# Kernel optimization log

Measured on AMD Instinct MI355X. Metric: run time of the kernel, lower is better.

## Reference

```python
import jax, jax.numpy as jnp
import numpy as np

N_HEAD = 16
QMIN, QMAX = 0.0, 255.0  # 8-bit asymmetric


def fake_quantize(x, scale, zp):
    # LearnableFakeQuantize (asymmetric, 8-bit) with straight-through round.
    q = x / scale + zp
    q = q + jax.lax.stop_gradient(jnp.round(q) - q)  # STE round
    q = jnp.clip(q, QMIN, QMAX)
    return (q - zp) * scale


def setup_inputs() -> dict:
    key = jax.random.key(0)
    ks = jax.random.split(key, 4)
    B, T, C = 2, 2048, 1024
    return {
        "hidden_states": jax.random.normal(ks[0], (B, T, C), jnp.float32),
        "W_attn": jax.random.normal(ks[1], (C, 3 * C), jnp.float32) * (1.0 / np.sqrt(C)),
        "b_attn": jnp.zeros((3 * C,), jnp.float32),
        "W_proj": jax.random.normal(ks[2], (C, C), jnp.float32) * (1.0 / np.sqrt(C)),
        "b_proj": jnp.zeros((C,), jnp.float32),
        "kv_scale": jnp.full((1,), 0.05, jnp.float32),
        "kv_zp": jnp.full((1,), 128.0, jnp.float32),
    }


def reference(hidden_states, W_attn, b_attn, W_proj, b_proj, kv_scale, kv_zp):
    B, T, C = hidden_states.shape
    H = N_HEAD
    D = C // H
    qkv = hidden_states @ W_attn + b_attn            # [B,T,3C]
    q, k, v = jnp.split(qkv, 3, axis=2)
    # [B,T,C] -> [B,H,T,D]
    q = q.reshape(B, T, H, D).transpose(0, 2, 1, 3)
    k = k.reshape(B, T, H, D).transpose(0, 2, 1, 3)
    v = v.reshape(B, T, H, D).transpose(0, 2, 1, 3)
    k = fake_quantize(k, kv_scale, kv_zp)
    v = fake_quantize(v, kv_scale, kv_zp)
    scores = jnp.einsum("bhqd,bhkd->bhqk", q, k) / jnp.sqrt(jnp.asarray(D, q.dtype))
    causal = jnp.tril(jnp.ones((T, T), bool))        # bias[:T,:T]
    scores = jnp.where(causal, scores, jnp.asarray(-jnp.inf, scores.dtype))
    attn = jax.nn.softmax(scores, axis=-1)
    out = jnp.einsum("bhqk,bhkd->bhqd", attn, v)     # [B,H,T,D]
    out = out.transpose(0, 2, 1, 3).reshape(B, T, C)
    return out @ W_proj + b_proj
```

## Files before the change

### kernel.cpp

```cpp
#include <hip/hip_runtime.h>
#include <math.h>

#define TB 2048
#define CC 1024
#define NH 16
#define HD 64

typedef __bf16 bf16x8 __attribute__((ext_vector_type(8)));
typedef __bf16 bf16x4 __attribute__((ext_vector_type(4)));
typedef float  f32x4  __attribute__((ext_vector_type(4)));

__device__ inline float exp2fast(float x) { return __builtin_amdgcn_exp2f(x); }

__device__ __forceinline__ void gl_lds16(const __bf16* g, __bf16* l) {
    __builtin_amdgcn_global_load_lds(
        (const __attribute__((address_space(1))) void*)g,
        (__attribute__((address_space(3))) void*)l, 16, 0, 0);
}

__global__ __launch_bounds__(256)
void prep_kernel(const float* __restrict__ hidden, __bf16* __restrict__ hb,
                 const float* __restrict__ Wa, __bf16* __restrict__ wat,
                 const float* __restrict__ Wp, __bf16* __restrict__ wpt)
{
    __shared__ __bf16 L[64][68];
    const int tid = threadIdx.x;
    const int bid = blockIdx.x;
    if (bid < 4096) {
        int i = (bid * 256 + tid) * 4;
        f32x4 v = *(const f32x4*)&hidden[i];
        bf16x4 o;
        o.x = (__bf16)v.x; o.y = (__bf16)v.y; o.z = (__bf16)v.z; o.w = (__bf16)v.w;
        *(bf16x4*)&hb[i] = o;
        return;
    }
    const float* src; __bf16* dst; int N, n0, k0;
    if (bid < 4096 + 768) {
        int t = bid - 4096;
        src = Wa; dst = wat; N = 3072;
        n0 = (t % 48) * 64; k0 = (t / 48) * 64;
    } else {
        int t = bid - 4864;
        src = Wp; dst = wpt; N = 1024;
        n0 = (t % 16) * 64; k0 = (t / 16) * 64;
    }
    #pragma unroll
    for (int i = 0; i < 4; i++) {
        int id = tid + i * 256;
        int r = id >> 4, c = (id & 15) * 4;
        f32x4 v = *(const f32x4*)&src[(size_t)(k0 + r) * N + n0 + c];
        bf16x4 o;
        o.x = (__bf16)v.x; o.y = (__bf16)v.y; o.z = (__bf16)v.z; o.w = (__bf16)v.w;
        *(bf16x4*)&L[r][c] = o;
    }
    __syncthreads();
    #pragma unroll
    for (int i = 0; i < 4; i++) {
        int id = tid + i * 256;
        int nr = id >> 4, kc = (id & 15) * 4;
        bf16x4 o;
        o.x = L[kc + 0][nr]; o.y = L[kc + 1][nr];
        o.z = L[kc + 2][nr]; o.w = L[kc + 3][nr];
        *(bf16x4*)&dst[(size_t)(n0 + nr) * 1024 + k0 + kc] = o;
    }
}

template<int BN, int MODE>
__global__ __launch_bounds__(256)
void gemm_bt(const __bf16* __restrict__ A, const __bf16* __restrict__ Bt,
             const float* __restrict__ bias,
             __bf16* __restrict__ o0, __bf16* __restrict__ o1,
             __bf16* __restrict__ o2, float* __restrict__ of,
             int M, int N, int K,
             const float* __restrict__ scp, const float* __restrict__ zpp)
{
    constexpr int NT = BN / 32;
    __shared__ __bf16 Asm[128][64];
    __shared__ __bf16 Bsm[BN][64];

    const int tid  = threadIdx.x;
    const int m0   = blockIdx.y * 128;
    const int n0   = blockIdx.x * BN;
    const int w    = tid >> 6, lane = tid & 63;
    const int wm   = (w & 1) * 64, wn = (w >> 1) * (BN / 2);
    const int r16  = lane & 15, quad = lane >> 4;
    const int srow = lane >> 3;
    const int scol = ((lane & 7) ^ srow) * 8;
    const int rsw  = r16 & 7;

    f32x4 acc[NT][4];
    #pragma unroll
    for (int i = 0; i < NT; i++)
        #pragma unroll
        for (int j = 0; j < 4; j++) acc[i][j] = 0.f;

    for (int k0 = 0; k0 < K; k0 += 64) {
        #pragma unroll
        for (int p = 0; p < 4; p++)
            gl_lds16(&A[(size_t)(m0 + w * 32 + p * 8 + srow) * K + k0 + scol],
                     &Asm[w * 32 + p * 8][0]);
        #pragma unroll
        for (int p = 0; p < BN / 32; p++)
            gl_lds16(&Bt[(size_t)(n0 + w * (BN / 4) + p * 8 + srow) * K + k0 + scol],
                     &Bsm[w * (BN / 4) + p * 8][0]);
        __syncthreads();

        #pragma unroll
        for (int ks = 0; ks < 2; ks++) {
            const int col = ((ks * 4 + quad) ^ rsw) * 8;
            bf16x8 af[4], bfr[NT];
            #pragma unroll
            for (int mt = 0; mt < 4; mt++)
                af[mt] = *(const bf16x8*)&Asm[wm + mt * 16 + r16][col];
            #pragma unroll
            for (int nt = 0; nt < NT; nt++)
                bfr[nt] = *(const bf16x8*)&Bsm[wn + nt * 16 + r16][col];
            #pragma unroll
            for (int nt = 0; nt < NT; nt++)
                #pragma unroll
                for (int mt = 0; mt < 4; mt++)
                    acc[nt][mt] = __builtin_amdgcn_mfma_f32_16x16x32_bf16(
                        bfr[nt], af[mt], acc[nt][mt], 0, 0, 0);
        }
        __syncthreads();
    }

    const float sc = scp[0];
    const float zp = zpp[0];

    #pragma unroll
    for (int nt = 0; nt < NT; nt++) {
        #pragma unroll
        for (int mt = 0; mt < 4; mt++) {
            int gm = m0 + wm + mt * 16 + r16;
            int gn = n0 + wn + nt * 16 + quad * 4;
            f32x4 val = acc[nt][mt] + *(const f32x4*)&bias[gn];
            if (MODE == 1) {
                *(f32x4*)&of[(size_t)gm * N + gn] = val;
            } else {
                int part = gn >> 10;
                int idx  = gn & 1023;
                int h = idx >> 6, d = idx & 63;
                int b = gm >> 11, t = gm & 2047;
                size_t off = (((size_t)(b * NH + h)) * TB + t) * HD + d;
                bf16x4 st;
                if (part == 0) {
                    #pragma unroll
                    for (int r = 0; r < 4; r++)
                        st[r] = (__bf16)(val[r] * 0.18033688f);
                    *(bf16x4*)&o0[off] = st;
                } else {
                    #pragma unroll
                    for (int r = 0; r < 4; r++) {
                        float qv = val[r] / sc + zp;
                        qv = rintf(qv);
                        qv = fminf(fmaxf(qv, 0.f), 255.f);
                        st[r] = (__bf16)((qv - zp) * sc);
                    }
                    if (part == 1) *(bf16x4*)&o1[off] = st;
                    else           *(bf16x4*)&o2[off] = st;
                }
            }
        }
    }
}

__global__ __launch_bounds__(256, 4)
void attn_mfma(const __bf16* __restrict__ Q, const __bf16* __restrict__ Kg,
               const __bf16* __restrict__ Vg, __bf16* __restrict__ O)
{
    __shared__ alignas(16) __bf16 Ksm[64][72];
    __shared__ alignas(16) __bf16 Vsm[64][72];

    const int tid  = threadIdx.x;
    const int qt   = 31 - (blockIdx.x >> 5);
    const int bh   = blockIdx.x & 31;
    const int q0   = qt * 64;
    const int w    = tid >> 6, lane = tid & 63;
    const int l15  = lane & 15, quad = lane >> 4;
    const int b    = bh >> 4, h = bh & 15;

    const int krow = tid >> 3;
    const int kseg = (tid & 7) * 8;
    const int vkey = tid & 63;
    const int vc   = tid >> 6;

    const __bf16* Kbh = Kg + (size_t)bh * TB * HD;
    const __bf16* Vbh = Vg + (size_t)bh * TB * HD;

    const __bf16* Qrow = Q + ((size_t)bh * TB + q0 + w * 16 + l15) * HD;
    bf16x8 qf0 = *(const bf16x8*)&Qrow[quad * 8];
    bf16x8 qf1 = *(const bf16x8*)&Qrow[32 + quad * 8];

    const int rbase = (l15 >> 2) * 8 + (l15 & 3);

    bf16x8 af_l;
    {
        __bf16 v = (l15 == 0) ? (__bf16)1.0f : (__bf16)0.0f;
        #pragma unroll
        for (int j = 0; j < 8; j++) af_l[j] = v;
    }

    f32x4 acc_o[4], acc_l;
    #pragma unroll
    for (int nt = 0; nt < 4; nt++) acc_o[nt] = 0.f;
    acc_l = 0.f;
    float mrun = -3.0e38f;

    bf16x8 kpre0 = *(const bf16x8*)&Kbh[(size_t)krow * HD + kseg];
    bf16x8 kpre1 = *(const bf16x8*)&Kbh[(size_t)(32 + krow) * HD + kseg];
    bf16x8 vpre0 = *(const bf16x8*)&Vbh[(size_t)vkey * HD + vc * 8];
    bf16x8 vpre1 = *(const bf16x8*)&Vbh[(size_t)vkey * HD + (4 + vc) * 8];

    for (int kt = 0; kt <= qt; kt++) {
        __syncthreads();
        *(bf16x8*)&Ksm[krow][kseg]      = kpre0;
        *(bf16x8*)&Ksm[32 + krow][kseg] = kpre1;
        #pragma unroll
        for (int j = 0; j < 8; j++) {
            Vsm[vc * 8 + j][vkey]      = vpre0[j];
            Vsm[32 + vc * 8 + j][vkey] = vpre1[j];
        }
        __syncthreads();

        if (kt < qt) {
            const __bf16* Kn = Kbh + (size_t)(kt + 1) * 64 * HD;
            const __bf16* Vn = Vbh + (size_t)(kt + 1) * 64 * HD;
            kpre0 = *(const bf16x8*)&Kn[(size_t)krow * HD + kseg];
            kpre1 = *(const bf16x8*)&Kn[(size_t)(32 + krow) * HD + kseg];
            vpre0 = *(const bf16x8*)&Vn[(size_t)vkey * HD + vc * 8];
            vpre1 = *(const bf16x8*)&Vn[(size_t)vkey * HD + (4 + vc) * 8];
        }

        const bool diag = (kt == qt);

        f32x4 s[4];
        #pragma unroll
        for (int nt = 0; nt < 4; nt++) s[nt] = 0.f;
        #pragma unroll
        for (int nt = 0; nt < 4; nt++) {
            if (diag && (nt & 1) && w < 2) continue;
            int row = rbase + (nt & 1) * 32 + ((nt >> 1) << 2);
            bf16x8 kf0 = *(const bf16x8*)&Ksm[row][quad * 8];
            bf16x8 kf1 = *(const bf16x8*)&Ksm[row][32 + quad * 8];
            s[nt] = __builtin_amdgcn_mfma_f32_16x16x32_bf16(kf0, qf0, s[nt], 0, 0, 0);
            s[nt] = __builtin_amdgcn_mfma_f32_16x16x32_bf16(kf1, qf1, s[nt], 0, 0, 0);
        }

        if (diag) {
            #pragma unroll
            for (int nt = 0; nt < 4; nt++) {
                int koff = (nt & 1) * 32 + ((nt >> 1) << 2) + quad * 8;
                #pragma unroll
                for (int r = 0; r < 4; r++)
                    if (koff + r > w * 16 + l15) s[nt][r] = -3.0e38f;
            }
        }

        float mx = s[0][0];
        #pragma unroll
        for (int nt = 0; nt < 4; nt++)
            #pragma unroll
            for (int r = 0; r < 4; r++) mx = fmaxf(mx, s[nt][r]);
        mx = fmaxf(mx, __shfl_xor(mx, 16));
        mx = fmaxf(mx, __shfl_xor(mx, 32));

        float mnew  = fmaxf(mrun, mx);
        float alpha = exp2fast(mrun - mnew);
        mrun = mnew;
        #pragma unroll
        for (int nt = 0; nt < 4; nt++)
            #pragma unroll
            for (int r = 0; r < 4; r++) acc_o[nt][r] *= alpha;
        acc_l[0] *= alpha;

        float p[4][4];
        #pragma unroll
        for (int nt = 0; nt < 4; nt++)
            #pragma unroll
            for (int r = 0; r < 4; r++) p[nt][r] = exp2fast(s[nt][r] - mnew);

        bf16x8 pf0, pf1;
        #pragma unroll
        for (int j = 0; j < 4; j++) {
            pf0[j]     = (__bf16)p[0][j];
            pf0[4 + j] = (__bf16)p[2][j];
            pf1[j]     = (__bf16)p[1][j];
            pf1[4 + j] = (__bf16)p[3][j];
        }

        acc_l = __builtin_amdgcn_mfma_f32_16x16x32_bf16(af_l, pf0, acc_l, 0, 0, 0);
        acc_l = __builtin_amdgcn_mfma_f32_16x16x32_bf16(af_l, pf1, acc_l, 0, 0, 0);

        #pragma unroll
        for (int nt = 0; nt < 4; nt++) {
            bf16x8 vf0 = *(const bf16x8*)&Vsm[nt * 16 + l15][quad * 8];
            bf16x8 vf1 = *(const bf16x8*)&Vsm[nt * 16 + l15][32 + quad * 8];
            acc_o[nt] = __builtin_amdgcn_mfma_f32_16x16x32_bf16(vf0, pf0, acc_o[nt], 0, 0, 0);
            acc_o[nt] = __builtin_amdgcn_mfma_f32_16x16x32_bf16(vf1, pf1, acc_o[nt], 0, 0, 0);
        }
    }

    float lall = __shfl(acc_l[0], l15);
    float inv  = 1.f / lall;
    size_t trow = (size_t)(b * TB) + q0 + w * 16 + l15;
    #pragma unroll
    for (int nt = 0; nt < 4; nt++) {
        bf16x4 st;
        #pragma unroll
        for (int r = 0; r < 4; r++) st[r] = (__bf16)(acc_o[nt][r] * inv);
        *(bf16x4*)&O[trow * CC + h * HD + nt * 16 + quad * 4] = st;
    }
}

extern "C" void kernel_launch(void* const* d_in, const int* in_sizes, int n_in,
                              void* d_out, int out_size, void* d_ws, size_t ws_size,
                              hipStream_t stream) {
    (void)in_sizes; (void)n_in; (void)out_size; (void)ws_size;
    const float* hidden   = (const float*)d_in[0];
    const float* W_attn   = (const float*)d_in[1];
    const float* b_attn   = (const float*)d_in[2];
    const float* W_proj   = (const float*)d_in[3];
    const float* b_proj   = (const float*)d_in[4];
    const float* kv_scale = (const float*)d_in[5];
    const float* kv_zp    = (const float*)d_in[6];
    float* out = (float*)d_out;

    __bf16* hb  = (__bf16*)d_ws;
    __bf16* wat = hb  + (size_t)4096 * 1024;
    __bf16* wpt = wat + (size_t)3072 * 1024;
    __bf16* qws = wpt + (size_t)1024 * 1024;
    __bf16* kws = qws + (size_t)2 * NH * TB * HD;
    __bf16* vws = kws + (size_t)2 * NH * TB * HD;
    __bf16* ows = vws + (size_t)2 * NH * TB * HD;

    prep_kernel<<<5120, 256, 0, stream>>>(hidden, hb, W_attn, wat, W_proj, wpt);

    gemm_bt<128, 0><<<dim3(24, 32), 256, 0, stream>>>(
        hb, wat, b_attn, qws, kws, vws, nullptr, 4096, 3072, 1024, kv_scale, kv_zp);

    attn_mfma<<<dim3(32 * 32), 256, 0, stream>>>(qws, kws, vws, ows);

    gemm_bt<64, 1><<<dim3(16, 32), 256, 0, stream>>>(
        ows, wpt, b_proj, nullptr, nullptr, nullptr, out, 4096, 1024, 1024,
        kv_scale, kv_zp);
}
```

Measured before the change: 182.6 us.

## Swizzle K/V shared tiles, skip small-max rescales, raise MFMA wave priority

Replaces the padded 64x72 K/V shared-memory tiles with unpadded 64x64 tiles using an XOR swizzle on 16-byte chunks, so reads and writes avoid bank conflicts while using less LDS. The online-softmax rescale of the accumulators now runs only when some lane's running max grows by more than 8 (in log2 units). Otherwise the stale max is kept, and p values can reach up to 2^8 before the bf16 conversion. Adds s_setprio around the MFMA sections so waves in those sections get issue priority. The lazy rescale risks overflow or precision loss if the tolerance is wrong.

```diff
diff --git a/kernel.cpp b/kernel.cpp
--- a/kernel.cpp
+++ b/kernel.cpp
@@ -165,12 +165,16 @@
     }
 }
 
+__device__ __forceinline__ int swz_row(int row) {
+    return (row & 7) ^ (((row >> 3) & 1) << 2);
+}
+
 __global__ __launch_bounds__(256, 4)
 void attn_mfma(const __bf16* __restrict__ Q, const __bf16* __restrict__ Kg,
                const __bf16* __restrict__ Vg, __bf16* __restrict__ O)
 {
-    __shared__ alignas(16) __bf16 Ksm[64][72];
-    __shared__ alignas(16) __bf16 Vsm[64][72];
+    __shared__ alignas(16) __bf16 Ksm[64][64];
+    __shared__ alignas(16) __bf16 Vsm[64][64];
 
     const int tid  = threadIdx.x;
     const int qt   = 31 - (blockIdx.x >> 5);
@@ -181,7 +185,8 @@
     const int b    = bh >> 4, h = bh & 15;
 
     const int krow = tid >> 3;
-    const int kseg = (tid & 7) * 8;
+    const int kseg = tid & 7;
+    const int kcol = (kseg ^ swz_row(krow)) * 8;
     const int vkey = tid & 63;
     const int vc   = tid >> 6;
 
@@ -207,27 +212,29 @@
     acc_l = 0.f;
     float mrun = -3.0e38f;
 
-    bf16x8 kpre0 = *(const bf16x8*)&Kbh[(size_t)krow * HD + kseg];
-    bf16x8 kpre1 = *(const bf16x8*)&Kbh[(size_t)(32 + krow) * HD + kseg];
+    bf16x8 kpre0 = *(const bf16x8*)&Kbh[(size_t)krow * HD + kseg * 8];
+    bf16x8 kpre1 = *(const bf16x8*)&Kbh[(size_t)(32 + krow) * HD + kseg * 8];
     bf16x8 vpre0 = *(const bf16x8*)&Vbh[(size_t)vkey * HD + vc * 8];
     bf16x8 vpre1 = *(const bf16x8*)&Vbh[(size_t)vkey * HD + (4 + vc) * 8];
 
     for (int kt = 0; kt <= qt; kt++) {
         __syncthreads();
-        *(bf16x8*)&Ksm[krow][kseg]      = kpre0;
-        *(bf16x8*)&Ksm[32 + krow][kseg] = kpre1;
+        *(bf16x8*)&Ksm[krow][kcol]      = kpre0;
+        *(bf16x8*)&Ksm[32 + krow][kcol] = kpre1;
         #pragma unroll
         for (int j = 0; j < 8; j++) {
-            Vsm[vc * 8 + j][vkey]      = vpre0[j];
-            Vsm[32 + vc * 8 + j][vkey] = vpre1[j];
+            int sw  = j ^ ((vc & 1) << 2);
+            int col = (((vkey >> 3) ^ sw) << 3) | (vkey & 7);
+            Vsm[vc * 8 + j][col]      = vpre0[j];
+            Vsm[32 + vc * 8 + j][col] = vpre1[j];
         }
         __syncthreads();
 
         if (kt < qt) {
             const __bf16* Kn = Kbh + (size_t)(kt + 1) * 64 * HD;
             const __bf16* Vn = Vbh + (size_t)(kt + 1) * 64 * HD;
-            kpre0 = *(const bf16x8*)&Kn[(size_t)krow * HD + kseg];
-            kpre1 = *(const bf16x8*)&Kn[(size_t)(32 + krow) * HD + kseg];
+            kpre0 = *(const bf16x8*)&Kn[(size_t)krow * HD + kseg * 8];
+            kpre1 = *(const bf16x8*)&Kn[(size_t)(32 + krow) * HD + kseg * 8];
             vpre0 = *(const bf16x8*)&Vn[(size_t)vkey * HD + vc * 8];
             vpre1 = *(const bf16x8*)&Vn[(size_t)vkey * HD + (4 + vc) * 8];
         }
@@ -237,15 +244,18 @@
         f32x4 s[4];
         #pragma unroll
         for (int nt = 0; nt < 4; nt++) s[nt] = 0.f;
+        __builtin_amdgcn_s_setprio(1);
         #pragma unroll
         for (int nt = 0; nt < 4; nt++) {
             if (diag && (nt & 1) && w < 2) continue;
             int row = rbase + (nt & 1) * 32 + ((nt >> 1) << 2);
-            bf16x8 kf0 = *(const bf16x8*)&Ksm[row][quad * 8];
-            bf16x8 kf1 = *(const bf16x8*)&Ksm[row][32 + quad * 8];
+            int sw  = swz_row(row);
+            bf16x8 kf0 = *(const bf16x8*)&Ksm[row][(quad ^ sw) * 8];
+            bf16x8 kf1 = *(const bf16x8*)&Ksm[row][((quad + 4) ^ sw) * 8];
             s[nt] = __builtin_amdgcn_mfma_f32_16x16x32_bf16(kf0, qf0, s[nt], 0, 0, 0);
             s[nt] = __builtin_amdgcn_mfma_f32_16x16x32_bf16(kf1, qf1, s[nt], 0, 0, 0);
         }
+        __builtin_amdgcn_s_setprio(0);
 
         if (diag) {
             #pragma unroll
@@ -257,28 +267,30 @@
             }
         }
 
-        float mx = s[0][0];
-        #pragma unroll
-        for (int nt = 0; nt < 4; nt++)
-            #pragma unroll
-            for (int r = 0; r < 4; r++) mx = fmaxf(mx, s[nt][r]);
+        float m0 = fmaxf(fmaxf(s[0][0], s[0][1]), fmaxf(s[0][2], s[0][3]));
+        float m1 = fmaxf(fmaxf(s[1][0], s[1][1]), fmaxf(s[1][2], s[1][3]));
+        float m2 = fmaxf(fmaxf(s[2][0], s[2][1]), fmaxf(s[2][2], s[2][3]));
+        float m3 = fmaxf(fmaxf(s[3][0], s[3][1]), fmaxf(s[3][2], s[3][3]));
+        float mx = fmaxf(fmaxf(m0, m1), fmaxf(m2, m3));
         mx = fmaxf(mx, __shfl_xor(mx, 16));
         mx = fmaxf(mx, __shfl_xor(mx, 32));
 
-        float mnew  = fmaxf(mrun, mx);
-        float alpha = exp2fast(mrun - mnew);
-        mrun = mnew;
+        if (__any((mx - mrun) > 8.0f)) {
+            float mnew  = fmaxf(mrun, mx);
+            float alpha = exp2fast(mrun - mnew);
+            mrun = mnew;
+            #pragma unroll
+            for (int nt = 0; nt < 4; nt++)
+                #pragma unroll
+                for (int r = 0; r < 4; r++) acc_o[nt][r] *= alpha;
+            acc_l[0] *= alpha;
+        }
+
+        float p[4][4];
         #pragma unroll
         for (int nt = 0; nt < 4; nt++)
             #pragma unroll
-            for (int r = 0; r < 4; r++) acc_o[nt][r] *= alpha;
-        acc_l[0] *= alpha;
-
-        float p[4][4];
-        #pragma unroll
-        for (int nt = 0; nt < 4; nt++)
-            #pragma unroll
-            for (int r = 0; r < 4; r++) p[nt][r] = exp2fast(s[nt][r] - mnew);
+            for (int r = 0; r < 4; r++) p[nt][r] = exp2fast(s[nt][r] - mrun);
 
         bf16x8 pf0, pf1;
         #pragma unroll
@@ -289,16 +301,20 @@
             pf1[4 + j] = (__bf16)p[3][j];
         }
 
+        __builtin_amdgcn_s_setprio(1);
         acc_l = __builtin_amdgcn_mfma_f32_16x16x32_bf16(af_l, pf0, acc_l, 0, 0, 0);
         acc_l = __builtin_amdgcn_mfma_f32_16x16x32_bf16(af_l, pf1, acc_l, 0, 0, 0);
 
         #pragma unroll
         for (int nt = 0; nt < 4; nt++) {
-            bf16x8 vf0 = *(const bf16x8*)&Vsm[nt * 16 + l15][quad * 8];
-            bf16x8 vf1 = *(const bf16x8*)&Vsm[nt * 16 + l15][32 + quad * 8];
+            int vrow = nt * 16 + l15;
+            int sw   = swz_row(vrow);
+            bf16x8 vf0 = *(const bf16x8*)&Vsm[vrow][(quad ^ sw) * 8];
+            bf16x8 vf1 = *(const bf16x8*)&Vsm[vrow][((quad + 4) ^ sw) * 8];
             acc_o[nt] = __builtin_amdgcn_mfma_f32_16x16x32_bf16(vf0, pf0, acc_o[nt], 0, 0, 0);
             acc_o[nt] = __builtin_amdgcn_mfma_f32_16x16x32_bf16(vf1, pf1, acc_o[nt], 0, 0, 0);
         }
+        __builtin_amdgcn_s_setprio(0);
     }
 
     float lall = __shfl(acc_l[0], l15);
```

Measured after the change: 190.7 us. +4.4%, slower.

## Pair complementary causal query tiles in one 512-thread attention block

Applied to the files above, without the earlier changes.

Each attention block now runs 8 waves: the first four handle query tile 31-p and the last four handle tile p, so both share one K/V tile stream in LDS and every block does the same total causal work. The grid is halved to 512 blocks, and each thread now loads a single K and V vector per tile instead of two. Waves on the shorter tile skip compute once they pass their diagonal but still join the barriers. MFMA sections are wrapped in s_setprio to favour matrix issue. The cost is larger blocks with some idle waves sitting at barriers, plus possible register or occupancy pressure from the 512-thread launch bound.

```diff
diff --git a/kernel.cpp b/kernel.cpp
--- a/kernel.cpp
+++ b/kernel.cpp
@@ -165,7 +165,7 @@
     }
 }
 
-__global__ __launch_bounds__(256, 4)
+__global__ __launch_bounds__(512, 4)
 void attn_mfma(const __bf16* __restrict__ Q, const __bf16* __restrict__ Kg,
                const __bf16* __restrict__ Vg, __bf16* __restrict__ O)
 {
@@ -173,10 +173,13 @@
     __shared__ alignas(16) __bf16 Vsm[64][72];
 
     const int tid  = threadIdx.x;
-    const int qt   = 31 - (blockIdx.x >> 5);
+    const int p    = blockIdx.x >> 5;
     const int bh   = blockIdx.x & 31;
+    const int w    = tid >> 6, lane = tid & 63;
+    const int wq   = w & 3;
+    const int qt   = (w < 4) ? (31 - p) : p;
+    const int ktmax = 31 - p;
     const int q0   = qt * 64;
-    const int w    = tid >> 6, lane = tid & 63;
     const int l15  = lane & 15, quad = lane >> 4;
     const int b    = bh >> 4, h = bh & 15;
 
@@ -188,7 +191,7 @@
     const __bf16* Kbh = Kg + (size_t)bh * TB * HD;
     const __bf16* Vbh = Vg + (size_t)bh * TB * HD;
 
-    const __bf16* Qrow = Q + ((size_t)bh * TB + q0 + w * 16 + l15) * HD;
+    const __bf16* Qrow = Q + ((size_t)bh * TB + q0 + wq * 16 + l15) * HD;
     bf16x8 qf0 = *(const bf16x8*)&Qrow[quad * 8];
     bf16x8 qf1 = *(const bf16x8*)&Qrow[32 + quad * 8];
 
@@ -207,45 +210,42 @@
     acc_l = 0.f;
     float mrun = -3.0e38f;
 
-    bf16x8 kpre0 = *(const bf16x8*)&Kbh[(size_t)krow * HD + kseg];
-    bf16x8 kpre1 = *(const bf16x8*)&Kbh[(size_t)(32 + krow) * HD + kseg];
-    bf16x8 vpre0 = *(const bf16x8*)&Vbh[(size_t)vkey * HD + vc * 8];
-    bf16x8 vpre1 = *(const bf16x8*)&Vbh[(size_t)vkey * HD + (4 + vc) * 8];
-
-    for (int kt = 0; kt <= qt; kt++) {
+    bf16x8 kpre = *(const bf16x8*)&Kbh[(size_t)krow * HD + kseg];
+    bf16x8 vpre = *(const bf16x8*)&Vbh[(size_t)vkey * HD + vc * 8];
+
+    for (int kt = 0; kt <= ktmax; kt++) {
         __syncthreads();
-        *(bf16x8*)&Ksm[krow][kseg]      = kpre0;
-        *(bf16x8*)&Ksm[32 + krow][kseg] = kpre1;
-        #pragma unroll
-        for (int j = 0; j < 8; j++) {
-            Vsm[vc * 8 + j][vkey]      = vpre0[j];
-            Vsm[32 + vc * 8 + j][vkey] = vpre1[j];
-        }
+        *(bf16x8*)&Ksm[krow][kseg] = kpre;
+        #pragma unroll
+        for (int j = 0; j < 8; j++)
+            Vsm[vc * 8 + j][vkey] = vpre[j];
         __syncthreads();
 
-        if (kt < qt) {
+        if (kt < ktmax) {
             const __bf16* Kn = Kbh + (size_t)(kt + 1) * 64 * HD;
             const __bf16* Vn = Vbh + (size_t)(kt + 1) * 64 * HD;
-            kpre0 = *(const bf16x8*)&Kn[(size_t)krow * HD + kseg];
-            kpre1 = *(const bf16x8*)&Kn[(size_t)(32 + krow) * HD + kseg];
-            vpre0 = *(const bf16x8*)&Vn[(size_t)vkey * HD + vc * 8];
-            vpre1 = *(const bf16x8*)&Vn[(size_t)vkey * HD + (4 + vc) * 8];
-        }
+            kpre = *(const bf16x8*)&Kn[(size_t)krow * HD + kseg];
+            vpre = *(const bf16x8*)&Vn[(size_t)vkey * HD + vc * 8];
+        }
+
+        if (kt > qt) continue;
 
         const bool diag = (kt == qt);
 
         f32x4 s[4];
         #pragma unroll
         for (int nt = 0; nt < 4; nt++) s[nt] = 0.f;
+        __builtin_amdgcn_s_setprio(1);
         #pragma unroll
         for (int nt = 0; nt < 4; nt++) {
-            if (diag && (nt & 1) && w < 2) continue;
+            if (diag && (nt & 1) && wq < 2) continue;
             int row = rbase + (nt & 1) * 32 + ((nt >> 1) << 2);
             bf16x8 kf0 = *(const bf16x8*)&Ksm[row][quad * 8];
             bf16x8 kf1 = *(const bf16x8*)&Ksm[row][32 + quad * 8];
             s[nt] = __builtin_amdgcn_mfma_f32_16x16x32_bf16(kf0, qf0, s[nt], 0, 0, 0);
             s[nt] = __builtin_amdgcn_mfma_f32_16x16x32_bf16(kf1, qf1, s[nt], 0, 0, 0);
         }
+        __builtin_amdgcn_s_setprio(0);
 
         if (diag) {
             #pragma unroll
@@ -253,15 +253,15 @@
                 int koff = (nt & 1) * 32 + ((nt >> 1) << 2) + quad * 8;
                 #pragma unroll
                 for (int r = 0; r < 4; r++)
-                    if (koff + r > w * 16 + l15) s[nt][r] = -3.0e38f;
+                    if (koff + r > wq * 16 + l15) s[nt][r] = -3.0e38f;
             }
         }
 
-        float mx = s[0][0];
-        #pragma unroll
-        for (int nt = 0; nt < 4; nt++)
-            #pragma unroll
-            for (int r = 0; r < 4; r++) mx = fmaxf(mx, s[nt][r]);
+        float m0 = fmaxf(fmaxf(s[0][0], s[0][1]), fmaxf(s[0][2], s[0][3]));
+        float m1 = fmaxf(fmaxf(s[1][0], s[1][1]), fmaxf(s[1][2], s[1][3]));
+        float m2 = fmaxf(fmaxf(s[2][0], s[2][1]), fmaxf(s[2][2], s[2][3]));
+        float m3 = fmaxf(fmaxf(s[3][0], s[3][1]), fmaxf(s[3][2], s[3][3]));
+        float mx = fmaxf(fmaxf(m0, m1), fmaxf(m2, m3));
         mx = fmaxf(mx, __shfl_xor(mx, 16));
         mx = fmaxf(mx, __shfl_xor(mx, 32));
 
@@ -274,21 +274,22 @@
             for (int r = 0; r < 4; r++) acc_o[nt][r] *= alpha;
         acc_l[0] *= alpha;
 
-        float p[4][4];
+        float pv[4][4];
         #pragma unroll
         for (int nt = 0; nt < 4; nt++)
             #pragma unroll
-            for (int r = 0; r < 4; r++) p[nt][r] = exp2fast(s[nt][r] - mnew);
+            for (int r = 0; r < 4; r++) pv[nt][r] = exp2fast(s[nt][r] - mnew);
 
         bf16x8 pf0, pf1;
         #pragma unroll
         for (int j = 0; j < 4; j++) {
-            pf0[j]     = (__bf16)p[0][j];
-            pf0[4 + j] = (__bf16)p[2][j];
-            pf1[j]     = (__bf16)p[1][j];
-            pf1[4 + j] = (__bf16)p[3][j];
-        }
-
+            pf0[j]     = (__bf16)pv[0][j];
+            pf0[4 + j] = (__bf16)pv[2][j];
+            pf1[j]     = (__bf16)pv[1][j];
+            pf1[4 + j] = (__bf16)pv[3][j];
+        }
+
+        __builtin_amdgcn_s_setprio(1);
         acc_l = __builtin_amdgcn_mfma_f32_16x16x32_bf16(af_l, pf0, acc_l, 0, 0, 0);
         acc_l = __builtin_amdgcn_mfma_f32_16x16x32_bf16(af_l, pf1, acc_l, 0, 0, 0);
 
@@ -299,11 +300,12 @@
             acc_o[nt] = __builtin_amdgcn_mfma_f32_16x16x32_bf16(vf0, pf0, acc_o[nt], 0, 0, 0);
             acc_o[nt] = __builtin_amdgcn_mfma_f32_16x16x32_bf16(vf1, pf1, acc_o[nt], 0, 0, 0);
         }
+        __builtin_amdgcn_s_setprio(0);
     }
 
     float lall = __shfl(acc_l[0], l15);
     float inv  = 1.f / lall;
-    size_t trow = (size_t)(b * TB) + q0 + w * 16 + l15;
+    size_t trow = (size_t)(b * TB) + q0 + wq * 16 + l15;
     #pragma unroll
     for (int nt = 0; nt < 4; nt++) {
         bf16x4 st;
@@ -339,7 +341,7 @@
     gemm_bt<128, 0><<<dim3(24, 32), 256, 0, stream>>>(
         hb, wat, b_attn, qws, kws, vws, nullptr, 4096, 3072, 1024, kv_scale, kv_zp);
 
-    attn_mfma<<<dim3(32 * 32), 256, 0, stream>>>(qws, kws, vws, ows);
+    attn_mfma<<<dim3(16 * 32), 512, 0, stream>>>(qws, kws, vws, ows);
 
     gemm_bt<64, 1><<<dim3(16, 32), 256, 0, stream>>>(
         ows, wpt, b_proj, nullptr, nullptr, nullptr, out, 4096, 1024, 1024,
```

Result: no change. 180.6 us (-1.1%).
